# Optimization experiments

Hardware: AMD Instinct MI355X
Metric: run time of the kernel (lower is better)

## Reference

```python
import jax, jax.numpy as jnp
import numpy as np

N_NODES = 50000
N_EDGES = 800000
IN_FEATURES = 256
HIDDEN = 128


def setup_inputs() -> dict:
    key = jax.random.key(0)
    k_x, k_r, k_c, k_v, k_w, k_b = jax.random.split(key, 6)
    x = jax.random.normal(k_x, (N_NODES, IN_FEATURES), dtype=jnp.float32)
    adj_row = jax.random.randint(k_r, (N_EDGES,), 0, N_NODES, dtype=jnp.int32)
    adj_col = jax.random.randint(k_c, (N_EDGES,), 0, N_NODES, dtype=jnp.int32)
    adj_val = jax.random.uniform(k_v, (N_EDGES,), dtype=jnp.float32)
    # Linear params: weight [hidden, in_features] (xavier-normal-ish), bias [hidden]
    std = float(np.sqrt(2.0 / (IN_FEATURES + HIDDEN)))
    W = jax.random.normal(k_w, (HIDDEN, IN_FEATURES), dtype=jnp.float32) * std
    b = jax.random.normal(k_b, (HIDDEN,), dtype=jnp.float32) * 0.01
    return {"x": x, "adj_row": adj_row, "adj_col": adj_col, "adj_val": adj_val, "W": W, "b": b}


def reference(x, adj_row, adj_col, adj_val, W, b):
    # support = Linear(x): [N, hidden]
    support = jnp.einsum('nf,hf->nh', x, W) + b
    # sparse adj @ support via edge-list gather + segment-sum scatter
    gathered = support[adj_col] * adj_val[:, None]          # [E, hidden]
    out = jax.ops.segment_sum(gathered, adj_row, num_segments=N_NODES)  # [N, hidden]
    return out
```

## Files before the change

### kernel.cpp

```cpp
#include <hip/hip_runtime.h>

#define N_NODES 50000
#define N_EDGES 800000
#define IN_F    256
#define HIDDEN  128

#define BUCKET_SZ 64
#define NB        782
#define NBINS     1024
#define EBLOCK    3328
#define EPT       13
#define EBLOCKS   241
#define LIN_ROWS  64
#define LBLOCKS   782
#define NTASKS    1023
#define OFST_W    256
#define CAP       1300
#define NFRAG     4096

#define SMEM_BYTES 35840

typedef __attribute__((ext_vector_type(8))) short bf16x8;
typedef __attribute__((ext_vector_type(4))) float f32x4;

__device__ inline unsigned short f2bf(float f) {
    unsigned u = __float_as_uint(f);
    u += 0x7FFF + ((u >> 16) & 1);
    return (unsigned short)(u >> 16);
}
__device__ inline bf16x8 cvt8(float4 a, float4 b) {
    bf16x8 r;
    r[0] = (short)f2bf(a.x); r[1] = (short)f2bf(a.y);
    r[2] = (short)f2bf(a.z); r[3] = (short)f2bf(a.w);
    r[4] = (short)f2bf(b.x); r[5] = (short)f2bf(b.y);
    r[6] = (short)f2bf(b.z); r[7] = (short)f2bf(b.w);
    return r;
}
__device__ inline float bfLo(unsigned u) { return __uint_as_float(u << 16); }
__device__ inline float bfHi(unsigned u) { return __uint_as_float(u & 0xFFFF0000u); }

__global__ __launch_bounds__(256) void wconv_kernel(
    const float* __restrict__ W, unsigned short* __restrict__ wb)
{
    const int f = blockIdx.x * 256 + threadIdx.x;
    if (f >= NFRAG) return;
    const int ln = f & 63;
    const int s  = (f >> 6) & 7;
    const int hk = f >> 9;
    const int row = s * 16 + (ln & 15);
    const int k0  = hk * 32 + (ln >> 4) * 8;
    const float* wp = W + (size_t)row * IN_F + k0;
    float4 b0 = *(const float4*)wp;
    float4 b1 = *(const float4*)(wp + 4);
    *(bf16x8*)(wb + (size_t)f * 8) = cvt8(b0, b1);
}

__global__ __launch_bounds__(256, 4) void fused_linear_partition_kernel(
    const float* __restrict__ x, const unsigned short* __restrict__ wb,
    const float* __restrict__ bias, unsigned short* __restrict__ support,
    const int* __restrict__ adj_row, const int* __restrict__ adj_col,
    const float* __restrict__ adj_val,
    int2* __restrict__ part, int* __restrict__ ofsT)
{
    const int tid = threadIdx.x;

    if (blockIdx.x < EBLOCKS) {
        __shared__ __align__(16) char smem[SMEM_BYTES];
        int2* lbuf = (int2*)smem;
        int*  lofs = (int*)(smem + 26624);
        int*  lcur = (int*)(smem + 30720);
        int*  wsm  = (int*)(smem + 34816);

        const int task = blockIdx.x;
        const int base = task * EBLOCK;
        const int n    = min(EBLOCK, N_EDGES - base);
        const int lane = tid & 63;
        const int wv   = tid >> 6;

        for (int i = tid; i < NBINS; i += 256) lofs[i] = 0;
        __syncthreads();

        unsigned pk[EPT]; float pv[EPT];
#pragma unroll
        for (int i = 0; i < EPT; ++i) {
            int li = tid + i * 256;
            bool ok = li < n;
            int ee = ok ? (base + li) : base;
            int r = adj_row[ee], c = adj_col[ee];
            float v = adj_val[ee];
            if (ok) {
                unsigned bk = (unsigned)r >> 6;
                pk[i] = (bk << 22) | (((unsigned)r & 63u) << 16) | (unsigned)c;
                pv[i] = v;
                atomicAdd(&lofs[bk], 1);
            } else pk[i] = 0xFFFFFFFFu;
        }
        __syncthreads();

        int s0 = lofs[tid * 4], s1 = lofs[tid * 4 + 1];
        int s2 = lofs[tid * 4 + 2], s3 = lofs[tid * 4 + 3];
        int mysum = s0 + s1 + s2 + s3;
        int iv = mysum;
#pragma unroll
        for (int off = 1; off < 64; off <<= 1) {
            int t = __shfl_up(iv, off);
            if (lane >= off) iv += t;
        }
        if (lane == 63) wsm[wv] = iv;
        __syncthreads();
        int wpre = 0;
#pragma unroll
        for (int w = 0; w < 4; ++w) {
            int sw = wsm[w];
            if (w < wv) wpre += sw;
        }
        int ex = wpre + iv - mysum;
        lofs[tid * 4]     = ex;
        lofs[tid * 4 + 1] = ex + s0;
        lofs[tid * 4 + 2] = ex + s0 + s1;
        lofs[tid * 4 + 3] = ex + s0 + s1 + s2;
        __syncthreads();

        for (int i = tid; i < NBINS; i += 256) lcur[i] = lofs[i];
        __syncthreads();

#pragma unroll
        for (int i = 0; i < EPT; ++i) {
            if (pk[i] != 0xFFFFFFFFu) {
                unsigned bk = pk[i] >> 22;
                int p = atomicAdd(&lcur[bk], 1);
                lbuf[p] = make_int2((int)(pk[i] & 0x3FFFFF), __float_as_int(pv[i]));
            }
        }
        __syncthreads();

        for (int j = tid; j < n; j += 256)
            part[(size_t)task * EBLOCK + j] = lbuf[j];
        for (int i = tid; i <= NB; i += 256)
            ofsT[(size_t)i * OFST_W + task] = lofs[i];
    } else {
        const int bid  = blockIdx.x - EBLOCKS;
        const int lane = tid & 63;
        const int wave = tid >> 6;
        const int quad = lane >> 4;
        const int l16  = lane & 15;

        int m = bid * LIN_ROWS + wave * 16 + l16;
        if (m >= N_NODES) m = N_NODES - 1;
        const float* xrow = x + (size_t)m * IN_F;
        const bf16x8* wbv = (const bf16x8*)wb;

        f32x4 acc[8];
#pragma unroll
        for (int s = 0; s < 8; ++s) acc[s] = (f32x4){0.f, 0.f, 0.f, 0.f};

#pragma unroll 2
        for (int hk = 0; hk < 8; ++hk) {
            const int k0 = hk * 32 + quad * 8;
            float4 a0 = *(const float4*)(xrow + k0);
            float4 a1 = *(const float4*)(xrow + k0 + 4);
            bf16x8 af = cvt8(a0, a1);
            const bf16x8* bb = wbv + (size_t)hk * 512 + lane;
#pragma unroll
            for (int s = 0; s < 8; ++s) {
                bf16x8 bf = bb[(size_t)s * 64];
                acc[s] = __builtin_amdgcn_mfma_f32_16x16x32_bf16(af, bf, acc[s], 0, 0, 0);
            }
        }

        const int rowBase = bid * LIN_ROWS + wave * 16 + quad * 4;
#pragma unroll
        for (int reg = 0; reg < 4; ++reg) {
            const int r = rowBase + reg;
            if (r < N_NODES) {
#pragma unroll
                for (int s = 0; s < 8; ++s) {
                    const int col = s * 16 + l16;
                    float v = acc[s][reg] + bias[col];
                    support[(size_t)r * HIDDEN + col] = f2bf(v);
                }
            }
        }
    }
}

__global__ __launch_bounds__(512) void bucket_gather_kernel(
    const int* __restrict__ ofsT, const int2* __restrict__ part,
    const unsigned int* __restrict__ support_u32, float* __restrict__ out)
{
    __shared__ int2 sbufA[CAP];
    __shared__ int2 sbufB[CAP];
    __shared__ int  wsum[8];
    __shared__ int  hist[BUCKET_SZ];
    __shared__ int  rp[BUCKET_SZ + 1];
    __shared__ int  cur[BUCKET_SZ];

    const int tid  = threadIdx.x;
    const int b    = blockIdx.x;
    const int wave = tid >> 6;
    const int lane = tid & 63;

    if (tid < BUCKET_SZ) hist[tid] = 0;

    int s0 = 0, slen = 0;
    if (tid < EBLOCKS) {
        s0   = ofsT[(size_t)b * OFST_W + tid];
        slen = ofsT[(size_t)(b + 1) * OFST_W + tid] - s0;
    }

    int iv = slen;
#pragma unroll
    for (int off = 1; off < 64; off <<= 1) {
        int t = __shfl_up(iv, off);
        if (lane >= off) iv += t;
    }
    if (lane == 63) wsum[wave] = iv;
    __syncthreads();
    int wpre = 0, total = 0;
#pragma unroll
    for (int w = 0; w < 8; ++w) {
        int sw = wsum[w];
        total += sw;
        if (w < wave) wpre += sw;
    }
    const int excl = wpre + iv - slen;
    const int n    = min(total, CAP);

    {
        const int2* seg = part + (size_t)tid * EBLOCK + s0;
        for (int k = 0; k < slen; ++k) {
            int p = excl + k;
            if (p < CAP) {
                int2 cv = seg[k];
                sbufA[p] = cv;
                atomicAdd(&hist[(cv.x >> 16) & 63], 1);
            }
        }
    }
    __syncthreads();

    if (tid < 64) {
        int a = hist[tid];
        int ia = a;
#pragma unroll
        for (int off = 1; off < 64; off <<= 1) {
            int t = __shfl_up(ia, off);
            if (tid >= off) ia += t;
        }
        rp[tid + 1] = ia;
        if (tid == 0) rp[0] = 0;
        cur[tid] = ia - a;
    }
    __syncthreads();

    for (int j = tid; j < n; j += 512) {
        int2 cv = sbufA[j];
        int p = atomicAdd(&cur[(cv.x >> 16) & 63], 1);
        sbufB[p] = cv;
    }
    __syncthreads();

    const int q   = lane >> 4;
    const int l16 = lane & 15;
    const uint4* support4 = (const uint4*)support_u32;
    const int rowLo = wave * 8;
#pragma unroll 1
    for (int r = rowLo; r < rowLo + 8; ++r) {
        const int grow = b * BUCKET_SZ + r;
        if (grow >= N_NODES) break;
        const int s = rp[r], e = rp[r + 1];
        float a0 = 0.f, a1 = 0.f, a2 = 0.f, a3 = 0.f;
        float a4 = 0.f, a5 = 0.f, a6 = 0.f, a7 = 0.f;
        for (int j = s; j < e; j += 16) {
            int iA = j + q,      icA = min(iA, e - 1);
            int iB = j + 4 + q,  icB = min(iB, e - 1);
            int iC = j + 8 + q,  icC = min(iC, e - 1);
            int iD = j + 12 + q, icD = min(iD, e - 1);
            int2 cA = sbufB[icA];
            int2 cB = sbufB[icB];
            int2 cC = sbufB[icC];
            int2 cD = sbufB[icD];
            float vA = (iA < e) ? __int_as_float(cA.y) : 0.f;
            float vB = (iB < e) ? __int_as_float(cB.y) : 0.f;
            float vC = (iC < e) ? __int_as_float(cC.y) : 0.f;
            float vD = (iD < e) ? __int_as_float(cD.y) : 0.f;
            uint4 uA = support4[(size_t)(cA.x & 0xFFFF) * 16 + l16];
            uint4 uB = support4[(size_t)(cB.x & 0xFFFF) * 16 + l16];
            uint4 uC = support4[(size_t)(cC.x & 0xFFFF) * 16 + l16];
            uint4 uD = support4[(size_t)(cD.x & 0xFFFF) * 16 + l16];

            a0 += vA * bfLo(uA.x); a1 += vA * bfHi(uA.x);
            a2 += vA * bfLo(uA.y); a3 += vA * bfHi(uA.y);
            a4 += vA * bfLo(uA.z); a5 += vA * bfHi(uA.z);
            a6 += vA * bfLo(uA.w); a7 += vA * bfHi(uA.w);
            a0 += vB * bfLo(uB.x); a1 += vB * bfHi(uB.x);
            a2 += vB * bfLo(uB.y); a3 += vB * bfHi(uB.y);
            a4 += vB * bfLo(uB.z); a5 += vB * bfHi(uB.z);
            a6 += vB * bfLo(uB.w); a7 += vB * bfHi(uB.w);
            a0 += vC * bfLo(uC.x); a1 += vC * bfHi(uC.x);
            a2 += vC * bfLo(uC.y); a3 += vC * bfHi(uC.y);
            a4 += vC * bfLo(uC.z); a5 += vC * bfHi(uC.z);
            a6 += vC * bfLo(uC.w); a7 += vC * bfHi(uC.w);
            a0 += vD * bfLo(uD.x); a1 += vD * bfHi(uD.x);
            a2 += vD * bfLo(uD.y); a3 += vD * bfHi(uD.y);
            a4 += vD * bfLo(uD.z); a5 += vD * bfHi(uD.z);
            a6 += vD * bfLo(uD.w); a7 += vD * bfHi(uD.w);
        }
        a0 += __shfl_xor(a0, 16); a0 += __shfl_xor(a0, 32);
        a1 += __shfl_xor(a1, 16); a1 += __shfl_xor(a1, 32);
        a2 += __shfl_xor(a2, 16); a2 += __shfl_xor(a2, 32);
        a3 += __shfl_xor(a3, 16); a3 += __shfl_xor(a3, 32);
        a4 += __shfl_xor(a4, 16); a4 += __shfl_xor(a4, 32);
        a5 += __shfl_xor(a5, 16); a5 += __shfl_xor(a5, 32);
        a6 += __shfl_xor(a6, 16); a6 += __shfl_xor(a6, 32);
        a7 += __shfl_xor(a7, 16); a7 += __shfl_xor(a7, 32);
        float s0v, s1v;
        if      (q == 0) { s0v = a0; s1v = a1; }
        else if (q == 1) { s0v = a2; s1v = a3; }
        else if (q == 2) { s0v = a4; s1v = a5; }
        else             { s0v = a6; s1v = a7; }
        *(float2*)(out + (size_t)grow * HIDDEN + l16 * 8 + q * 2) = make_float2(s0v, s1v);
    }
}

extern "C" void kernel_launch(void* const* d_in, const int* in_sizes, int n_in,
                              void* d_out, int out_size, void* d_ws, size_t ws_size,
                              hipStream_t stream) {
    const float* x       = (const float*)d_in[0];
    const int*   adj_row = (const int*)d_in[1];
    const int*   adj_col = (const int*)d_in[2];
    const float* adj_val = (const float*)d_in[3];
    const float* W       = (const float*)d_in[4];
    const float* b       = (const float*)d_in[5];
    float* out = (float*)d_out;

    char* wsb = (char*)d_ws;
    const size_t off_support = 0;
    const size_t off_part    = off_support + (size_t)N_NODES * HIDDEN * 2;
    const size_t off_ofsT    = off_part + (size_t)EBLOCKS * EBLOCK * 8;
    const size_t off_wb      = off_ofsT + (size_t)(NB + 1) * OFST_W * 4;

    unsigned short* support = (unsigned short*)(wsb + off_support);
    int2* part = (int2*)(wsb + off_part);
    int*  ofsT = (int*)(wsb + off_ofsT);
    unsigned short* wb = (unsigned short*)(wsb + off_wb);

    wconv_kernel<<<NFRAG / 256, 256, 0, stream>>>(W, wb);
    fused_linear_partition_kernel<<<NTASKS, 256, 0, stream>>>(
        x, wb, b, support, adj_row, adj_col, adj_val, part, ofsT);
    bucket_gather_kernel<<<NB, 512, 0, stream>>>(
        ofsT, part, (const unsigned int*)support, out);
}
```

Measured before the change: 156.3 us.

## Halve row bucket size and shrink edge partition blocks for more gather blocks

Row buckets shrink from 64 to 32 rows, doubling the number of gather blocks to 1563, and the gather kernel drops from 512 to 256 threads. Each thread now merges two partition segments, and the inner loop is unrolled two ways instead of four. Edge partition blocks shrink to 2048 edges, giving 391 partition blocks. The goal is more parallelism and occupancy in the gather phase. In exchange it adds more partition blocks, a wider offset table, and less memory-level parallelism per thread in the gather loop.

After: 162.1 us. 1.04x slower.

```diff
diff --git a/kernel.cpp b/kernel.cpp
--- a/kernel.cpp
+++ b/kernel.cpp
@@ -5,20 +5,20 @@
 #define IN_F    256
 #define HIDDEN  128
 
-#define BUCKET_SZ 64
-#define NB        782
-#define NBINS     1024
-#define EBLOCK    3328
-#define EPT       13
-#define EBLOCKS   241
+#define BUCKET_SZ 32
+#define NB        1563
+#define NBINS     2048
+#define EBLOCK    2048
+#define EPT       8
+#define EBLOCKS   391
 #define LIN_ROWS  64
 #define LBLOCKS   782
-#define NTASKS    1023
-#define OFST_W    256
-#define CAP       1300
+#define NTASKS    1173
+#define OFST_W    400
+#define CAP       768
 #define NFRAG     4096
 
-#define SMEM_BYTES 35840
+#define SMEM_BYTES 32800
 
 typedef __attribute__((ext_vector_type(8))) short bf16x8;
 typedef __attribute__((ext_vector_type(4))) float f32x4;
@@ -67,9 +67,9 @@
     if (blockIdx.x < EBLOCKS) {
         __shared__ __align__(16) char smem[SMEM_BYTES];
         int2* lbuf = (int2*)smem;
-        int*  lofs = (int*)(smem + 26624);
-        int*  lcur = (int*)(smem + 30720);
-        int*  wsm  = (int*)(smem + 34816);
+        int*  lofs = (int*)(smem + 16384);
+        int*  lcur = (int*)(smem + 24576);
+        int*  wsm  = (int*)(smem + 32768);
 
         const int task = blockIdx.x;
         const int base = task * EBLOCK;
@@ -89,17 +89,17 @@
             int r = adj_row[ee], c = adj_col[ee];
             float v = adj_val[ee];
             if (ok) {
-                unsigned bk = (unsigned)r >> 6;
-                pk[i] = (bk << 22) | (((unsigned)r & 63u) << 16) | (unsigned)c;
+                unsigned bk = (unsigned)r >> 5;
+                pk[i] = (bk << 21) | (((unsigned)r & 31u) << 16) | (unsigned)c;
                 pv[i] = v;
                 atomicAdd(&lofs[bk], 1);
             } else pk[i] = 0xFFFFFFFFu;
         }
         __syncthreads();
 
-        int s0 = lofs[tid * 4], s1 = lofs[tid * 4 + 1];
-        int s2 = lofs[tid * 4 + 2], s3 = lofs[tid * 4 + 3];
-        int mysum = s0 + s1 + s2 + s3;
+        int sv[8]; int mysum = 0;
+#pragma unroll
+        for (int i = 0; i < 8; ++i) { sv[i] = lofs[tid * 8 + i]; mysum += sv[i]; }
         int iv = mysum;
 #pragma unroll
         for (int off = 1; off < 64; off <<= 1) {
@@ -114,11 +114,9 @@
             int sw = wsm[w];
             if (w < wv) wpre += sw;
         }
-        int ex = wpre + iv - mysum;
-        lofs[tid * 4]     = ex;
-        lofs[tid * 4 + 1] = ex + s0;
-        lofs[tid * 4 + 2] = ex + s0 + s1;
-        lofs[tid * 4 + 3] = ex + s0 + s1 + s2;
+        int run = wpre + iv - mysum;
+#pragma unroll
+        for (int i = 0; i < 8; ++i) { int t = sv[i]; lofs[tid * 8 + i] = run; run += t; }
         __syncthreads();
 
         for (int i = tid; i < NBINS; i += 256) lcur[i] = lofs[i];
@@ -127,9 +125,9 @@
 #pragma unroll
         for (int i = 0; i < EPT; ++i) {
             if (pk[i] != 0xFFFFFFFFu) {
-                unsigned bk = pk[i] >> 22;
+                unsigned bk = pk[i] >> 21;
                 int p = atomicAdd(&lcur[bk], 1);
-                lbuf[p] = make_int2((int)(pk[i] & 0x3FFFFF), __float_as_int(pv[i]));
+                lbuf[p] = make_int2((int)(pk[i] & 0x1FFFFF), __float_as_int(pv[i]));
             }
         }
         __syncthreads();
@@ -184,13 +182,13 @@
     }
 }
 
-__global__ __launch_bounds__(512) void bucket_gather_kernel(
+__global__ __launch_bounds__(256) void bucket_gather_kernel(
     const int* __restrict__ ofsT, const int2* __restrict__ part,
     const unsigned int* __restrict__ support_u32, float* __restrict__ out)
 {
     __shared__ int2 sbufA[CAP];
     __shared__ int2 sbufB[CAP];
-    __shared__ int  wsum[8];
+    __shared__ int  wsum[4];
     __shared__ int  hist[BUCKET_SZ];
     __shared__ int  rp[BUCKET_SZ + 1];
     __shared__ int  cur[BUCKET_SZ];
@@ -202,11 +200,19 @@
 
     if (tid < BUCKET_SZ) hist[tid] = 0;
 
-    int s0 = 0, slen = 0;
+    const int* orow0 = ofsT + (size_t)b * OFST_W;
+    const int* orow1 = ofsT + (size_t)(b + 1) * OFST_W;
+    int s0 = 0, l0 = 0, s1 = 0, l1 = 0;
     if (tid < EBLOCKS) {
-        s0   = ofsT[(size_t)b * OFST_W + tid];
-        slen = ofsT[(size_t)(b + 1) * OFST_W + tid] - s0;
-    }
+        s0 = orow0[tid];
+        l0 = orow1[tid] - s0;
+    }
+    const int t2 = tid + 256;
+    if (t2 < EBLOCKS) {
+        s1 = orow0[t2];
+        l1 = orow1[t2] - s1;
+    }
+    const int slen = l0 + l1;
 
     int iv = slen;
 #pragma unroll
@@ -218,7 +224,7 @@
     __syncthreads();
     int wpre = 0, total = 0;
 #pragma unroll
-    for (int w = 0; w < 8; ++w) {
+    for (int w = 0; w < 4; ++w) {
         int sw = wsum[w];
         total += sw;
         if (w < wave) wpre += sw;
@@ -227,23 +233,32 @@
     const int n    = min(total, CAP);
 
     {
-        const int2* seg = part + (size_t)tid * EBLOCK + s0;
-        for (int k = 0; k < slen; ++k) {
+        const int2* seg0 = part + (size_t)tid * EBLOCK + s0;
+        for (int k = 0; k < l0; ++k) {
             int p = excl + k;
             if (p < CAP) {
-                int2 cv = seg[k];
+                int2 cv = seg0[k];
                 sbufA[p] = cv;
-                atomicAdd(&hist[(cv.x >> 16) & 63], 1);
+                atomicAdd(&hist[(cv.x >> 16) & 31], 1);
+            }
+        }
+        const int2* seg1 = part + (size_t)t2 * EBLOCK + s1;
+        for (int k = 0; k < l1; ++k) {
+            int p = excl + l0 + k;
+            if (p < CAP) {
+                int2 cv = seg1[k];
+                sbufA[p] = cv;
+                atomicAdd(&hist[(cv.x >> 16) & 31], 1);
             }
         }
     }
     __syncthreads();
 
-    if (tid < 64) {
+    if (tid < BUCKET_SZ) {
         int a = hist[tid];
         int ia = a;
 #pragma unroll
-        for (int off = 1; off < 64; off <<= 1) {
+        for (int off = 1; off < 32; off <<= 1) {
             int t = __shfl_up(ia, off);
             if (tid >= off) ia += t;
         }
@@ -253,9 +268,9 @@
     }
     __syncthreads();
 
-    for (int j = tid; j < n; j += 512) {
+    for (int j = tid; j < n; j += 256) {
         int2 cv = sbufA[j];
-        int p = atomicAdd(&cur[(cv.x >> 16) & 63], 1);
+        int p = atomicAdd(&cur[(cv.x >> 16) & 31], 1);
         sbufB[p] = cv;
     }
     __syncthreads();
@@ -271,23 +286,15 @@
         const int s = rp[r], e = rp[r + 1];
         float a0 = 0.f, a1 = 0.f, a2 = 0.f, a3 = 0.f;
         float a4 = 0.f, a5 = 0.f, a6 = 0.f, a7 = 0.f;
-        for (int j = s; j < e; j += 16) {
-            int iA = j + q,      icA = min(iA, e - 1);
-            int iB = j + 4 + q,  icB = min(iB, e - 1);
-            int iC = j + 8 + q,  icC = min(iC, e - 1);
-            int iD = j + 12 + q, icD = min(iD, e - 1);
+        for (int j = s; j < e; j += 8) {
+            int iA = j + q,     icA = min(iA, e - 1);
+            int iB = j + 4 + q, icB = min(iB, e - 1);
             int2 cA = sbufB[icA];
             int2 cB = sbufB[icB];
-            int2 cC = sbufB[icC];
-            int2 cD = sbufB[icD];
             float vA = (iA < e) ? __int_as_float(cA.y) : 0.f;
             float vB = (iB < e) ? __int_as_float(cB.y) : 0.f;
-            float vC = (iC < e) ? __int_as_float(cC.y) : 0.f;
-            float vD = (iD < e) ? __int_as_float(cD.y) : 0.f;
             uint4 uA = support4[(size_t)(cA.x & 0xFFFF) * 16 + l16];
             uint4 uB = support4[(size_t)(cB.x & 0xFFFF) * 16 + l16];
-            uint4 uC = support4[(size_t)(cC.x & 0xFFFF) * 16 + l16];
-            uint4 uD = support4[(size_t)(cD.x & 0xFFFF) * 16 + l16];
 
             a0 += vA * bfLo(uA.x); a1 += vA * bfHi(uA.x);
             a2 += vA * bfLo(uA.y); a3 += vA * bfHi(uA.y);
@@ -297,14 +304,6 @@
             a2 += vB * bfLo(uB.y); a3 += vB * bfHi(uB.y);
             a4 += vB * bfLo(uB.z); a5 += vB * bfHi(uB.z);
             a6 += vB * bfLo(uB.w); a7 += vB * bfHi(uB.w);
-            a0 += vC * bfLo(uC.x); a1 += vC * bfHi(uC.x);
-            a2 += vC * bfLo(uC.y); a3 += vC * bfHi(uC.y);
-            a4 += vC * bfLo(uC.z); a5 += vC * bfHi(uC.z);
-            a6 += vC * bfLo(uC.w); a7 += vC * bfHi(uC.w);
-            a0 += vD * bfLo(uD.x); a1 += vD * bfHi(uD.x);
-            a2 += vD * bfLo(uD.y); a3 += vD * bfHi(uD.y);
-            a4 += vD * bfLo(uD.z); a5 += vD * bfHi(uD.z);
-            a6 += vD * bfLo(uD.w); a7 += vD * bfHi(uD.w);
         }
         a0 += __shfl_xor(a0, 16); a0 += __shfl_xor(a0, 32);
         a1 += __shfl_xor(a1, 16); a1 += __shfl_xor(a1, 32);
@@ -348,6 +347,6 @@
     wconv_kernel<<<NFRAG / 256, 256, 0, stream>>>(W, wb);
     fused_linear_partition_kernel<<<NTASKS, 256, 0, stream>>>(
         x, wb, b, support, adj_row, adj_col, adj_val, part, ofsT);
-    bucket_gather_kernel<<<NB, 512, 0, stream>>>(
+    bucket_gather_kernel<<<NB, 256, 0, stream>>>(
         ofsT, part, (const unsigned int*)support, out);
 }
```
